# Optimization experiments

Hardware: AMD Instinct MI355X
Metric: run time of the kernel (lower is better)

Reference implementation:

```python
import jax, jax.numpy as jnp
import numpy as np

THRESHOLD = 0.5
DECAY = 0.95


def setup_inputs() -> dict:
    key = jax.random.key(0)
    x = jax.random.normal(key, (64, 1024, 512), dtype=jnp.float32)
    return {"x": x}


def reference(x):
    # x: [batch, seq_len, features]
    m0 = jnp.zeros(x[:, 0, :].shape, dtype=x.dtype)  # membrane potential [B, F]

    def step(m, xt):
        m = DECAY * m + xt                      # leaky integrate
        s = (m > THRESHOLD).astype(x.dtype)     # fire
        m = m * (1.0 - s)                       # reset fired neurons
        return m, s

    # scan over time (leading axis)
    _, spikes = jax.lax.scan(step, m0, jnp.swapaxes(x, 0, 1))  # [S, B, F]
    return jnp.swapaxes(spikes, 0, 1)  # [B, S, F]
```

## Files before the change

kernel.cpp:

```cpp
#include <hip/hip_runtime.h>


#define BATCH 64
#define SEQ   1024
#define FEAT  512
#define CHUNK 64

#define LOAD_CHUNK(buf, t0)                                              \
    {                                                                    \
        const float* __restrict__ xn = xp + (size_t)(t0) * FEAT;         \
        _Pragma("unroll")                                                \
        for (int u = 0; u < CHUNK; ++u) buf[u] = xn[(size_t)u * FEAT];   \
    }

#define COMPUTE_CHUNK(buf, t0)                                           \
    {                                                                    \
        float* __restrict__ on = op + (size_t)(t0) * FEAT;               \
        _Pragma("unroll")                                                \
        for (int u = 0; u < CHUNK; ++u) {                                \
            m = __fadd_rn(__fmul_rn(0.95f, m), buf[u]);                  \
            const bool fired = (m > 0.5f);                               \
            __builtin_nontemporal_store(fired ? 1.0f : 0.0f,             \
                                        &on[(size_t)u * FEAT]);          \
            m = fired ? 0.0f : m;                                        \
        }                                                                \
    }

__global__ __launch_bounds__(64, 1)
void lif_kernel(const float* __restrict__ x, float* __restrict__ out) {
    const int tid = blockIdx.x * blockDim.x + threadIdx.x;
    const int b = tid >> 9;
    const int f = tid & (FEAT - 1);
    const size_t base = (size_t)b * SEQ * FEAT + f;
    const float* __restrict__ xp = x + base;
    float* __restrict__ op = out + base;

    float m = 0.0f;
    float bufA[CHUNK], bufB[CHUNK];

    LOAD_CHUNK(bufA, 0)

    for (int t0 = 0; t0 < SEQ; t0 += 2 * CHUNK) {
        LOAD_CHUNK(bufB, t0 + CHUNK)
        COMPUTE_CHUNK(bufA, t0)
        if (t0 + 2 * CHUNK < SEQ) {
            LOAD_CHUNK(bufA, t0 + 2 * CHUNK)
        }
        COMPUTE_CHUNK(bufB, t0 + CHUNK)
    }
}

extern "C" void kernel_launch(void* const* d_in, const int* in_sizes, int n_in,
                              void* d_out, int out_size, void* d_ws, size_t ws_size,
                              hipStream_t stream) {
    const float* x = (const float*)d_in[0];
    float* out = (float*)d_out;
    const int total_threads = BATCH * FEAT;
    const int block = 64;
    const int grid = total_threads / block;
    lif_kernel<<<grid, block, 0, stream>>>(x, out);
}
```

Baseline: 46.18 us.

## Add prefetch blocks that stream input into cache alongside compute blocks

Launches 1536 extra single-wave blocks beside the 512 compute blocks. Each extra block reads a contiguous slice of the input with 16-byte vector loads and discards the sum, which is meant to pull the whole tensor into the large on-die cache before the serial scan threads ask for it. The intent is to hide the latency of the compute threads' strided per-timestep loads. In exchange it doubles read traffic, risks evicting lines before they are used, and depends on the prefetch blocks being scheduled early.

```diff
diff --git a/kernel.cpp b/kernel.cpp
--- a/kernel.cpp
+++ b/kernel.cpp
@@ -5,6 +5,11 @@
 #define SEQ   1024
 #define FEAT  512
 #define CHUNK 64
+#define NCOMPUTE  512
+#define NPREFETCH 1536
+#define UNITS (BATCH * SEQ * FEAT * 4 / 1024)
+
+typedef float f32x4 __attribute__((ext_vector_type(4)));
 
 #define LOAD_CHUNK(buf, t0)                                              \
     {                                                                    \
@@ -28,7 +33,27 @@
 
 __global__ __launch_bounds__(64, 1)
 void lif_kernel(const float* __restrict__ x, float* __restrict__ out) {
-    const int tid = blockIdx.x * blockDim.x + threadIdx.x;
+    const int bid  = blockIdx.x;
+    const int lane = threadIdx.x;
+
+    if (bid >= NCOMPUTE) {
+        const int p   = bid - NCOMPUTE;
+        const int per = (UNITS + NPREFETCH - 1) / NPREFETCH;
+        const char* __restrict__ xc = reinterpret_cast<const char*>(x);
+        float acc = 0.0f;
+        for (int i = 0; i < per; ++i) {
+            const int u = p * per + i;
+            if (u < UNITS) {
+                const f32x4 v = *reinterpret_cast<const f32x4*>(
+                    xc + (size_t)u * 1024 + (size_t)lane * 16);
+                acc += v.x + v.y + v.z + v.w;
+            }
+        }
+        asm volatile("" ::"v"(acc));
+        return;
+    }
+
+    const int tid = bid * 64 + lane;
     const int b = tid >> 9;
     const int f = tid & (FEAT - 1);
     const size_t base = (size_t)b * SEQ * FEAT + f;
@@ -55,8 +80,6 @@
                               hipStream_t stream) {
     const float* x = (const float*)d_in[0];
     float* out = (float*)d_out;
-    const int total_threads = BATCH * FEAT;
-    const int block = 64;
-    const int grid = total_threads / block;
-    lif_kernel<<<grid, block, 0, stream>>>(x, out);
+    const int grid = NCOMPUTE + NPREFETCH;
+    lif_kernel<<<grid, 64, 0, stream>>>(x, out);
 }
```

New measurement: 63.84 us. 1.38x slower.

## Split time axis into segments with speculative zero-state pass and repair pass

Applied to the files above, without the earlier changes.

Splits the sequence into four time segments computed in parallel from a zero initial membrane state, storing each segment's end state in workspace. A second kernel then replays each later segment from the true carried state and stops once a spike coincides with a speculative spike, since both trajectories reset to zero there and converge. This gives four times as many independent chains to hide memory latency, at the cost of a second launch and extra rereads of input and output until the two trajectories converge. It keeps a single-pass fallback for when the workspace is too small.

```diff
diff --git a/kernel.cpp b/kernel.cpp
--- a/kernel.cpp
+++ b/kernel.cpp
@@ -5,6 +5,10 @@
 #define SEQ   1024
 #define FEAT  512
 #define CHUNK 64
+#define NTB   4
+#define TBL   (SEQ / NTB)
+#define NCHAIN (BATCH * FEAT)
+#define PCHUNK 32
 
 #define LOAD_CHUNK(buf, t0)                                              \
     {                                                                    \
@@ -27,25 +31,86 @@
     }
 
 __global__ __launch_bounds__(64, 1)
-void lif_kernel(const float* __restrict__ x, float* __restrict__ out) {
-    const int tid = blockIdx.x * blockDim.x + threadIdx.x;
+void lif_pass1(const float* __restrict__ x, float* __restrict__ out,
+               float* __restrict__ ws) {
+    const int bid  = blockIdx.x;
+    const int lane = threadIdx.x;
+    const int cb = bid & 511;
+    const int tb = bid >> 9;
+    const int b  = cb >> 3;
+    const int f0 = (cb & 7) << 6;
+    const size_t base = (size_t)b * SEQ * FEAT + f0 + lane
+                      + (size_t)tb * TBL * FEAT;
+    const float* __restrict__ xp = x + base;
+    float* __restrict__ op = out + base;
+
+    float m = 0.0f;
+    float bufA[CHUNK], bufB[CHUNK];
+    LOAD_CHUNK(bufA, 0)
+    for (int t0 = 0; t0 < TBL; t0 += 2 * CHUNK) {
+        LOAD_CHUNK(bufB, t0 + CHUNK)
+        COMPUTE_CHUNK(bufA, t0)
+        if (t0 + 2 * CHUNK < TBL) LOAD_CHUNK(bufA, t0 + 2 * CHUNK)
+        COMPUTE_CHUNK(bufB, t0 + CHUNK)
+    }
+    if (tb < NTB - 1) ws[tb * NCHAIN + (cb << 6) + lane] = m;
+}
+
+__global__ __launch_bounds__(64, 1)
+void lif_pass2(const float* __restrict__ x, float* __restrict__ out,
+               const float* __restrict__ ws) {
+    const int cb   = blockIdx.x;
+    const int lane = threadIdx.x;
+    const int b  = cb >> 3;
+    const int f0 = (cb & 7) << 6;
+    const size_t base = (size_t)b * SEQ * FEAT + f0 + lane;
+    const float* __restrict__ xp = x + base;
+    float* __restrict__ op = out + base;
+    const int idx = (cb << 6) + lane;
+
+    float m = ws[idx];
+    for (int tb = 1; tb < NTB; ++tb) {
+        const int tbase = tb * TBL;
+        bool done = false;
+        for (int c0 = 0; c0 < TBL; c0 += PCHUNK) {
+            if (__all(done)) break;
+            float xb[PCHUNK], sb[PCHUNK];
+#pragma unroll
+            for (int u = 0; u < PCHUNK; ++u) {
+                xb[u] = xp[(size_t)(tbase + c0 + u) * FEAT];
+                sb[u] = op[(size_t)(tbase + c0 + u) * FEAT];
+            }
+#pragma unroll
+            for (int u = 0; u < PCHUNK; ++u) {
+                if (!done) {
+                    m = __fadd_rn(__fmul_rn(0.95f, m), xb[u]);
+                    const bool fired = (m > 0.5f);
+                    op[(size_t)(tbase + c0 + u) * FEAT] = fired ? 1.0f : 0.0f;
+                    const bool p1 = (sb[u] != 0.0f);
+                    if (fired) m = 0.0f;
+                    if (fired && p1) done = true;
+                }
+            }
+        }
+        if (done && tb < NTB - 1) m = ws[tb * NCHAIN + idx];
+    }
+}
+
+__global__ __launch_bounds__(64, 1)
+void lif_fallback(const float* __restrict__ x, float* __restrict__ out) {
+    const int tid = blockIdx.x * 64 + threadIdx.x;
     const int b = tid >> 9;
     const int f = tid & (FEAT - 1);
     const size_t base = (size_t)b * SEQ * FEAT + f;
     const float* __restrict__ xp = x + base;
     float* __restrict__ op = out + base;
-
     float m = 0.0f;
     float bufA[CHUNK], bufB[CHUNK];
-
     LOAD_CHUNK(bufA, 0)
-
     for (int t0 = 0; t0 < SEQ; t0 += 2 * CHUNK) {
         LOAD_CHUNK(bufB, t0 + CHUNK)
         COMPUTE_CHUNK(bufA, t0)
-        if (t0 + 2 * CHUNK < SEQ) {
-            LOAD_CHUNK(bufA, t0 + 2 * CHUNK)
-        }
+        if (t0 + 2 * CHUNK < SEQ) LOAD_CHUNK(bufA, t0 + 2 * CHUNK)
         COMPUTE_CHUNK(bufB, t0 + CHUNK)
     }
 }
@@ -55,8 +120,11 @@
                               hipStream_t stream) {
     const float* x = (const float*)d_in[0];
     float* out = (float*)d_out;
-    const int total_threads = BATCH * FEAT;
-    const int block = 64;
-    const int grid = total_threads / block;
-    lif_kernel<<<grid, block, 0, stream>>>(x, out);
+    const size_t ws_needed = (size_t)(NTB - 1) * NCHAIN * sizeof(float);
+    if (ws_size >= ws_needed) {
+        lif_pass1<<<NTB * 512, 64, 0, stream>>>(x, out, (float*)d_ws);
+        lif_pass2<<<512, 64, 0, stream>>>(x, out, (const float*)d_ws);
+    } else {
+        lif_fallback<<<512, 64, 0, stream>>>(x, out);
+    }
 }
```

Measured after the change: 101.7 us. 2.2x slower.
